# Kernel optimization log

Measured on AMD Instinct MI355X. Metric: run time of the kernel, lower is better.

## Reference

```python
import jax, jax.numpy as jnp
import numpy as np

B, L, D = 4, 1536, 768
H, DQK, DV = 8, 64, 96
NPF = 96  # num_pos_feats = (DV // (2*3)) * (2*3)


def pos_feats_exponential(positions, feature_size, seq_length, min_half_life=3.0):
    # positions: (P, 1); returns (P, feature_size)
    max_range = jnp.log(seq_length) / jnp.log(2.0)
    half_life = jnp.power(2.0, jnp.linspace(min_half_life, max_range, feature_size))
    return jnp.exp(-jnp.log(2.0) / half_life * jnp.abs(positions))


def pos_feats_central_mask(positions, feature_size):
    center_widths = jnp.power(2.0, jnp.arange(1, feature_size + 1, dtype=jnp.float32)) - 1.0
    return (center_widths > jnp.abs(positions)).astype(jnp.float32)


def pos_feats_gamma(positions, feature_size, seq_length):
    stddev = seq_length / (2.0 * feature_size)
    start_mean = seq_length / feature_size
    mean = jnp.linspace(start_mean, seq_length, feature_size)
    concentration = (mean / stddev) ** 2
    rate = mean / (stddev ** 2)
    x = jnp.abs(positions)
    log_unnorm = jax.scipy.special.xlogy(concentration - 1.0, x) - rate * x
    log_norm = jax.scipy.special.gammaln(concentration) - concentration * jnp.log(rate)
    probs = jnp.exp(log_unnorm - log_norm) + 1e-8
    return probs / jnp.max(probs, axis=0, keepdims=True)


def pos_feats_all(positions, feature_size, seq_length, symmetric=False):
    # 3 feature functions; if asymmetric, each is doubled by a signed copy
    num_basis = feature_size // 6
    emb = jnp.concatenate([
        pos_feats_exponential(positions, num_basis, seq_length),
        pos_feats_central_mask(positions, num_basis),
        pos_feats_gamma(positions, num_basis, seq_length),
    ], axis=-1)
    if not symmetric:
        emb = jnp.concatenate([emb, jnp.sign(positions) * emb], axis=-1)
    return emb  # (P, feature_size)


def relative_shift(x):
    # x: (b, h, t1, 2*t1 - 1) -> (b, h, t1, t1), Transformer-XL shift trick
    b, h, t1, t2 = x.shape
    x = jnp.concatenate([jnp.zeros_like(x[..., :1]), x], axis=-1)  # pad -> width t2+1 == 2*t1
    x = x.reshape(b, h, t2 + 1, t1)[:, :, 1:, :]
    x = x.reshape(b, h, t1, t2)
    return x[..., : (t2 + 2) // 2]


def setup_inputs() -> dict:
    key = jax.random.key(0)
    ks = jax.random.split(key, 9)

    def vs(k, shape):  # VarianceScaling(scale=2.0), fan_in on leading dim for 2D
        fan_in = shape[0] if len(shape) == 2 else shape[-1]
        return jax.random.normal(k, shape, jnp.float32) * np.float32(np.sqrt(2.0 / fan_in))

    return {
        "x": jax.random.normal(ks[0], (B, L, D), jnp.float32),
        "Q_w": vs(ks[1], (D, H * DQK)),
        "K_w": vs(ks[2], (D, H * DQK)),
        "V_w": vs(ks[3], (D, H * DV)),
        "out_w": vs(ks[4], (D, H * DV)),
        "out_b": jnp.zeros((H * DV,), jnp.float32),
        "rel_K_w": vs(ks[5], (NPF, H * DQK)),
        "r_w_bias": vs(ks[6], (1, H, 1, DQK)),
        "r_r_bias": vs(ks[7], (1, H, 1, DQK)),
    }


def reference(x, Q_w, K_w, V_w, out_w, out_b, rel_K_w, r_w_bias, r_r_bias):
    b, l, d = x.shape
    h = r_w_bias.shape[1]
    dqk = Q_w.shape[1] // h

    def heads(w, inp):
        out = inp @ w  # (b, t, h*dh)
        return out.reshape(inp.shape[0], inp.shape[1], h, -1).transpose(0, 2, 1, 3)

    Q = heads(Q_w, x) * (dqk ** -0.5)  # scaling=True
    K = heads(K_w, x)
    V = heads(V_w, x)

    positions = jnp.arange(1 - l, l, dtype=jnp.float32)[:, None]       # (2l-1, 1)
    pe = pos_feats_all(positions, rel_K_w.shape[0], float(l))           # (2l-1, npf)
    r_K = (pe @ rel_K_w).reshape(2 * l - 1, h, dqk).transpose(1, 0, 2)  # (h, 2l-1, dqk)

    content = jnp.einsum('bhid,bhjd->bhij', Q + r_w_bias, K)            # (b, h, l, l)
    rel = jnp.einsum('bhid,hjd->bhij', Q + r_r_bias, r_K)               # (b, h, l, 2l-1)
    logits = content + relative_shift(rel)

    w = jax.nn.softmax(logits, axis=-1)
    attn = jnp.einsum('bhij,bhjd->bhid', w, V)                          # (b, h, l, dv)
    out = attn.transpose(0, 2, 1, 3).reshape(b, l, -1) @ out_w + out_b
    return out
```

## Files before the change

kernel.cpp:

```cpp
#include <hip/hip_runtime.h>


typedef unsigned short u16;
typedef unsigned int   u32;

typedef __bf16 bf16x8_t __attribute__((ext_vector_type(8)));
typedef unsigned short u16x8_t __attribute__((ext_vector_type(8)));
typedef float f32x4_t __attribute__((ext_vector_type(4)));

union Frag { u16x8_t u; bf16x8_t b; };

__device__ __forceinline__ float bf2f(u16 v){
  union { u32 i; float f; } c; c.i = ((u32)v) << 16; return c.f;
}
__device__ __forceinline__ u16 f2bf(float f){
  union { float f; u32 i; } c; c.f = f;
  u32 r = c.i + 0x7FFFu + ((c.i >> 16) & 1u);
  return (u16)(r >> 16);
}
__device__ __forceinline__ u16 f2bf_hw(float f){
  __bf16 h = (__bf16)f;
  union { __bf16 h; u16 u; } c; c.h = h; return c.u;
}
__device__ __forceinline__ float frcp(float x){
#if __has_builtin(__builtin_amdgcn_rcpf)
  return __builtin_amdgcn_rcpf(x);
#else
  return 1.0f / x;
#endif
}

template<int N>
__device__ __forceinline__ float ror16(float x){
  union { float f; int i; } c; c.f = x;
  int y = __builtin_amdgcn_update_dpp(0, c.i, 0x120 + N, 0xF, 0xF, true);
  union { int i; float f; } d; d.i = y;
  return d.f;
}
__device__ __forceinline__ float rowmax16(float v){
  v = fmaxf(v, ror16<1>(v));
  v = fmaxf(v, ror16<2>(v));
  v = fmaxf(v, ror16<4>(v));
  v = fmaxf(v, ror16<8>(v));
  return v;
}

#define GLB __attribute__((address_space(1)))
#define LDSAS __attribute__((address_space(3)))
__device__ __forceinline__ void async16(const void* g, void* l){
  __builtin_amdgcn_global_load_lds((const GLB u32*)g, (LDSAS u32*)l, 16, 0, 0);
}

#define LQ   1536
#define NPOS 3071
#define NPOSP 3072

__global__ __launch_bounds__(256) void pre_k(
    const float* __restrict__ x,
    const float* __restrict__ Qw_, const float* __restrict__ Kw_,
    const float* __restrict__ Vw_, const float* __restrict__ Ow_,
    const float* __restrict__ relKw,
    u16* __restrict__ xb, u16* __restrict__ WtQKV, u16* __restrict__ WtOut,
    u16* __restrict__ rK)
{
  const int bx = blockIdx.x;
  const int t = threadIdx.x;

  if (bx < 4608) {
    int gid = bx * 256 + t;
    float4 v = ((const float4*)x)[gid];
    xb[4*gid+0] = f2bf(v.x); xb[4*gid+1] = f2bf(v.y);
    xb[4*gid+2] = f2bf(v.z); xb[4*gid+3] = f2bf(v.w);
    return;
  }

  if (bx < 5088) {
    __shared__ u16 tile[64][65];
    int b2 = bx - 4608;
    const float* src; int stride, cl0, c0, k0; u16* dst;
    if (b2 < 336) {
      int ct = b2 % 28, kt = b2 / 28;
      c0 = ct*64; k0 = kt*64;
      if (c0 < 512)       { src = Qw_; stride = 512; cl0 = c0; }
      else if (c0 < 1024) { src = Kw_; stride = 512; cl0 = c0 - 512; }
      else                { src = Vw_; stride = 768; cl0 = c0 - 1024; }
      dst = WtQKV;
    } else {
      int b3 = b2 - 336; int ct = b3 % 12, kt = b3 / 12;
      c0 = ct*64; k0 = kt*64; src = Ow_; stride = 768; cl0 = c0; dst = WtOut;
    }
    #pragma unroll
    for (int e = 0; e < 16; ++e) {
      int idx = e*256 + t; int row = idx >> 6, col = idx & 63;
      tile[row][col] = f2bf(src[(size_t)(k0 + row)*stride + cl0 + col]);
    }
    __syncthreads();
    #pragma unroll
    for (int e = 0; e < 16; ++e) {
      int idx = e*256 + t; int orow = idx >> 6, ocol = idx & 63;
      dst[(size_t)(c0 + orow)*768 + k0 + ocol] = tile[ocol][orow];
    }
    return;
  }

  __shared__ float gmaxs[16];
  __shared__ float feats[4][96];
  const int k0 = (bx - 5088) * 4;

  if (t < 16) {
    float fi   = (float)(t + 1);
    float conc = 4.0f * fi * fi;
    float rate = fi / 24.0f;
    float c1   = conc - 1.0f;
    float lognorm = lgammaf(conc) - conc * logf(rate);
    float mode = 96.0f*fi - 24.0f/fi;
    float x1 = floorf(mode), x2 = x1 + 1.0f;
    if (x2 > 1535.0f) x2 = 1535.0f;
    float p1 = expf(c1*logf(x1) - rate*x1 - lognorm) + 1e-8f;
    float p2 = expf(c1*logf(x2) - rate*x2 - lognorm) + 1e-8f;
    gmaxs[t] = fmaxf(p1, p2);
  }
  __syncthreads();

  #pragma unroll
  for (int e = 0; e < 2; ++e) {
    int idx = e*256 + t;
    if (idx < 384) {
      int kl = idx / 96, f = idx - kl*96;
      int k = k0 + kl;
      float val = 0.0f;
      if (k != NPOS) {
        float pos = (float)(k - (LQ - 1));
        float xx  = fabsf(pos);
        float sgn = (float)((pos > 0.0f) - (pos < 0.0f));
        int fb = (f < 48) ? f : f - 48;
        float v;
        if (fb < 16) {
          float max_range = log2f((float)LQ);
          float hl = exp2f(3.0f + (float)fb * (max_range - 3.0f) / 15.0f);
          v = expf(-0.69314718056f / hl * xx);
        } else if (fb < 32) {
          int i = fb - 16;
          float width = (float)(1u << (i + 1)) - 1.0f;
          v = (width > xx) ? 1.0f : 0.0f;
        } else {
          int i = fb - 32;
          float fi   = (float)(i + 1);
          float conc = 4.0f * fi * fi;
          float rate = fi / 24.0f;
          float lognorm = lgammaf(conc) - conc * logf(rate);
          float lu = (xx == 0.0f) ? -INFINITY : ((conc - 1.0f) * logf(xx) - rate * xx);
          float p  = expf(lu - lognorm) + 1e-8f;
          v = p / gmaxs[i];
        }
        val = (f < 48) ? v : sgn * v;
      }
      feats[kl][f] = val;
    }
  }
  __syncthreads();

  #pragma unroll
  for (int ci = 0; ci < 2; ++ci) {
    int c = ci*256 + t;
    float a0 = 0.f, a1 = 0.f, a2 = 0.f, a3 = 0.f;
    #pragma unroll 4
    for (int f = 0; f < 96; ++f) {
      float wv = relKw[(size_t)f*512 + c];
      a0 += feats[0][f] * wv;
      a1 += feats[1][f] * wv;
      a2 += feats[2][f] * wv;
      a3 += feats[3][f] * wv;
    }
    size_t base = (((size_t)(c >> 6))*NPOSP + k0)*64 + (c & 63);
    rK[base +   0] = f2bf(a0);
    rK[base +  64] = f2bf(a1);
    rK[base + 128] = f2bf(a2);
    rK[base + 192] = f2bf(a3);
  }
}

__global__ __launch_bounds__(256) void qkv_gemm(
    const u16* __restrict__ xb, const u16* __restrict__ Wt,
    u16* __restrict__ Qb, u16* __restrict__ Kc, u16* __restrict__ Vt)
{
  const int n0 = blockIdx.x * 128;
  const int m0 = blockIdx.y * 128;
  const int tid = threadIdx.x, w = tid >> 6, lane = tid & 63, q = lane >> 4, s = lane & 15;
  const int wr = w >> 1, wc = w & 1;

  __shared__ __align__(16) u16 At[128*64];
  __shared__ __align__(16) u16 Bt[128*64];

  const char* ag = (const char*)(xb + (size_t)m0 * 768);
  const char* bg = (const char*)(Wt + (size_t)n0 * 768);

  const f32x4_t fz = {0.f, 0.f, 0.f, 0.f};
  f32x4_t acc[4][4];
  #pragma unroll
  for (int m = 0; m < 4; ++m)
    #pragma unroll
    for (int n = 0; n < 4; ++n) acc[m][n] = fz;

  for (int kk = 0; kk < 768; kk += 64) {
    #pragma unroll
    for (int c = 0; c < 4; ++c) {
      int ck = w*256 + c*64 + lane;
      int grow = ck >> 3, gcol = (ck & 7) ^ (grow & 7);
      async16(ag + (size_t)grow*1536 + (size_t)(kk + gcol*8)*2, &At[(size_t)(w*256 + c*64)*8]);
      async16(bg + (size_t)grow*1536 + (size_t)(kk + gcol*8)*2, &Bt[(size_t)(w*256 + c*64)*8]);
    }
    __syncthreads();
    #pragma unroll
    for (int kf = 0; kf < 2; ++kf) {
      int sw = (kf*4 + q) ^ (s & 7);
      Frag af[4], bf[4];
      #pragma unroll
      for (int m = 0; m < 4; ++m)
        af[m].u = *(const u16x8_t*)&At[(size_t)((wr*64 + m*16 + s)*8 + sw)*8];
      #pragma unroll
      for (int n = 0; n < 4; ++n)
        bf[n].u = *(const u16x8_t*)&Bt[(size_t)((wc*64 + n*16 + s)*8 + sw)*8];
      #pragma unroll
      for (int m = 0; m < 4; ++m)
        #pragma unroll
        for (int n = 0; n < 4; ++n)
          acc[m][n] = __builtin_amdgcn_mfma_f32_16x16x32_bf16(af[m].b, bf[n].b, acc[m][n], 0, 0, 0);
    }
    __syncthreads();
  }

  #pragma unroll
  for (int m = 0; m < 4; ++m) {
    #pragma unroll
    for (int n = 0; n < 4; ++n) {
      int c = n0 + wc*64 + n*16 + s;
      #pragma unroll
      for (int r = 0; r < 4; ++r) {
        int row = m0 + wr*64 + m*16 + q*4 + r;
        int b = row / LQ, i = row - b*LQ;
        float v = acc[m][n][r];
        if (c < 512) {
          int h = c >> 6, d = c & 63;
          Qb[(((size_t)(b*8 + h))*LQ + i)*64 + d] = f2bf(v * 0.125f);
        } else if (c < 1024) {
          int cc = c - 512, h = cc >> 6, d = cc & 63;
          Kc[(((size_t)(b*8 + h))*LQ + i)*64 + d] = f2bf(v);
        } else {
          int cc = c - 1024, h = cc / 96, vv = cc - h*96;
          Vt[(((size_t)(b*8 + h))*96 + vv)*LQ + i] = f2bf(v);
        }
      }
    }
  }
}

__global__ __launch_bounds__(512, 4) void attn_k(
    const u16* __restrict__ Qb, const u16* __restrict__ Kc,
    const u16* __restrict__ Vt, const u16* __restrict__ rK,
    const float* __restrict__ rwb, const float* __restrict__ rrb,
    u16* __restrict__ attnO, u16* __restrict__ Opart, float* __restrict__ ml,
    int nz)
{
  const int n = blockIdx.x;
  const int bpb = 12 * nz;
  const int slot = n >> 3;
  const int bh = (n & 7) * 4 + slot / bpb;
  const int rm = slot % bpb;
  const int it = rm % 12, z = rm / 12;
  const int i0 = it * 128;
  const int b = bh >> 3, h = bh & 7;
  const int tid = threadIdx.x;
  const int w = tid >> 6, lane = tid & 63, q = lane >> 4, s = lane & 15;

  __shared__ __align__(16) u16 Kt[64*64];
  __shared__ __align__(16) u16 Rt[256*64];
  __shared__ __align__(16) u16 Vs[96*64];
  __shared__ __align__(16) u16 Ps[8][16][72];

  Frag qwf[2], qrf[2];
  {
    const u16* qb = Qb + (((size_t)bh)*LQ + i0 + 16*w + s)*64;
    #pragma unroll
    for (int kf = 0; kf < 2; ++kf) {
      u16x8_t qraw = *(const u16x8_t*)(qb + kf*32 + q*8);
      #pragma unroll
      for (int j = 0; j < 8; ++j) {
        int d = kf*32 + q*8 + j;
        float qv = bf2f(qraw[j]);
        qwf[kf].u[j] = f2bf_hw(qv + rwb[h*64 + d]);
        qrf[kf].u[j] = f2bf_hw(qv + rrb[h*64 + d]);
      }
    }
  }

  Frag ones;
  #pragma unroll
  for (int j = 0; j < 8; ++j) ones.u[j] = 0x3F80;

  const f32x4_t fz = {0.f, 0.f, 0.f, 0.f};
  float mrun[4];
  f32x4_t acco[6], accl;
  #pragma unroll
  for (int r = 0; r < 4; ++r) mrun[r] = -1e30f;
  #pragma unroll
  for (int vs = 0; vs < 6; ++vs) acco[vs] = fz;
  accl = fz;

  const char* kcb = (const char*)(Kc + ((size_t)bh)*LQ*64);
  const char* vtb = (const char*)(Vt + ((size_t)bh)*96*LQ);
  const char* rkb = (const char*)(rK + ((size_t)h)*NPOSP*64);

  const int swz0 = (0*4 + q) ^ (s & 7);
  const int swz1 = (1*4 + q) ^ (s & 7);

  const int njt = 24 / nz;
  const int jt0 = z * njt;
  const int jtend = jt0 + njt;

  auto stageK = [&](int jtS) {
    const char* kg = kcb + (size_t)(jtS*64) * 128;
    int ck = tid;
    int grow = ck >> 3, gcol = (ck & 7) ^ (grow & 7);
    async16(kg + (size_t)grow*128 + gcol*16, &Kt[(size_t)(w*64)*8]);
  };
  auto stageV = [&](int jtS) {
    const char* vg = vtb + (size_t)(jtS*64) * 2;
    {
      int ck = tid;
      int grow = ck >> 3, gcol = (ck & 7) ^ (grow & 7);
      async16(vg + (size_t)grow*(LQ*2) + gcol*16, &Vs[(size_t)(w*64)*8]);
    }
    if (tid < 256) {
      int ck = 512 + tid;
      int grow = ck >> 3, gcol = (ck & 7) ^ (grow & 7);
      async16(vg + (size_t)grow*(LQ*2) + gcol*16, &Vs[(size_t)(512 + w*64)*8]);
    }
  };
  auto stageR64 = [&](int ar0) {
    const char* rg = rkb + (size_t)ar0 * 128;
    int ck = tid;
    int grow = ck >> 3, gcol = (ck & 7) ^ (grow & 7);
    async16(rg + (size_t)grow*128 + gcol*16, &Rt[(size_t)((ar0 & 255) + w*8)*64]);
  };

  {
    const int k00 = jt0*64 - i0 + (LQ - 128);
    stageK(jt0);
    stageR64(k00); stageR64(k00 + 64); stageR64(k00 + 128);
    stageV(jt0);
  }
  __syncthreads();

  for (int jt = jt0; jt < jtend; ++jt) {
    const int k0 = jt*64 - i0 + (LQ - 128);
    const int kb = k0 & 255;

    f32x4_t accc[4] = {fz, fz, fz, fz};
    f32x4_t accr[5] = {fz, fz, fz, fz, fz};
    #pragma unroll
    for (int ns = 0; ns < 4; ++ns) {
      int row = ns*16 + s;
      Frag b0; b0.u = *(const u16x8_t*)&Kt[(size_t)(row*8 + swz0)*8];
      Frag b1; b1.u = *(const u16x8_t*)&Kt[(size_t)(row*8 + swz1)*8];
      accc[ns] = __builtin_amdgcn_mfma_f32_16x16x32_bf16(qwf[0].b, b0.b, accc[ns], 0, 0, 0);
      accc[ns] = __builtin_amdgcn_mfma_f32_16x16x32_bf16(qwf[1].b, b1.b, accc[ns], 0, 0, 0);
    }
    #pragma unroll
    for (int nn = 0; nn < 5; ++nn) {
      int row = (kb + (7 - w + nn)*16 + s) & 255;
      Frag b0; b0.u = *(const u16x8_t*)&Rt[(size_t)(row*8 + swz0)*8];
      Frag b1; b1.u = *(const u16x8_t*)&Rt[(size_t)(row*8 + swz1)*8];
      accr[nn] = __builtin_amdgcn_mfma_f32_16x16x32_bf16(qrf[0].b, b0.b, accr[nn], 0, 0, 0);
      accr[nn] = __builtin_amdgcn_mfma_f32_16x16x32_bf16(qrf[1].b, b1.b, accr[nn], 0, 0, 0);
    }

    __syncthreads();

    if (jt + 1 < jtend) {
      stageK(jt + 1);
      stageR64(k0 + 192);
    }

    #pragma unroll
    for (int r = 0; r < 4; ++r) {
      int tt = s + 15 - 4*q - r;
      int srcl = (lane & 48) | (tt & 15);
      bool hi = tt >= 16;
      float v[5];
      #pragma unroll
      for (int nn = 0; nn < 5; ++nn) v[nn] = __shfl(accr[nn][r], srcl, 64);
      #pragma unroll
      for (int ns = 0; ns < 4; ++ns)
        accc[ns][r] += hi ? v[ns + 1] : v[ns];
    }

    #pragma unroll
    for (int r = 0; r < 4; ++r) {
      float mx = fmaxf(fmaxf(accc[0][r], accc[1][r]), fmaxf(accc[2][r], accc[3][r]));
      mx = rowmax16(mx);
      float mnew  = fmaxf(mrun[r], mx);
      float alpha = __expf(mrun[r] - mnew);
      #pragma unroll
      for (int ns = 0; ns < 4; ++ns)
        accc[ns][r] = __expf(accc[ns][r] - mnew);
      mrun[r] = mnew;
      accl[r] *= alpha;
      #pragma unroll
      for (int vs = 0; vs < 6; ++vs) acco[vs][r] *= alpha;
    }

    #pragma unroll
    for (int ns = 0; ns < 4; ++ns)
      #pragma unroll
      for (int r = 0; r < 4; ++r)
        Ps[w][q*4 + r][ns*16 + s] = f2bf_hw(accc[ns][r]);

    #pragma unroll
    for (int kf = 0; kf < 2; ++kf) {
      Frag pf; pf.u = *(const u16x8_t*)(&Ps[w][s][kf*32 + q*8]);
      int sw = kf ? swz1 : swz0;
      #pragma unroll
      for (int vs = 0; vs < 6; ++vs) {
        int row = vs*16 + s;
        Frag vf; vf.u = *(const u16x8_t*)&Vs[(size_t)(row*8 + sw)*8];
        acco[vs] = __builtin_amdgcn_mfma_f32_16x16x32_bf16(pf.b, vf.b, acco[vs], 0, 0, 0);
      }
      accl = __builtin_amdgcn_mfma_f32_16x16x32_bf16(pf.b, ones.b, accl, 0, 0, 0);
    }

    __syncthreads();

    if (jt + 1 < jtend) stageV(jt + 1);
  }

  if (nz == 1) {
    #pragma unroll
    for (int r = 0; r < 4; ++r) {
      float inv = frcp(accl[r]);
      int i = i0 + 16*w + q*4 + r;
      #pragma unroll
      for (int vs = 0; vs < 6; ++vs) {
        int v = vs*16 + s;
        attnO[((size_t)b*LQ + i)*768 + h*96 + v] = f2bf_hw(acco[vs][r] * inv);
      }
    }
  } else {
    #pragma unroll
    for (int vs = 0; vs < 6; ++vs) {
      int v = vs*16 + s;
      #pragma unroll
      for (int r = 0; r < 4; ++r) {
        int i = i0 + 16*w + q*4 + r;
        size_t rg = (size_t)(z*32 + bh)*LQ + i;
        Opart[rg*96 + v] = f2bf_hw(acco[vs][r]);
      }
    }
    if (s == 0) {
      #pragma unroll
      for (int r = 0; r < 4; ++r) {
        int i = i0 + 16*w + q*4 + r;
        size_t rg = (size_t)(z*32 + bh)*LQ + i;
        ml[rg*2 + 0] = mrun[r];
        ml[rg*2 + 1] = accl[r];
      }
    }
  }
}

__global__ void combine_k(const u16* __restrict__ Opart, const float* __restrict__ ml,
                          u16* __restrict__ attnO, int nz)
{
  int g = blockIdx.x * 256 + threadIdx.x;
  if (g >= 32*LQ*12) return;
  int vg = g % 12, row = g / 12;
  int v0 = vg * 8;
  int bh = row / LQ, i = row - bh*LQ;
  int b = bh >> 3, h = bh & 7;
  float M = -1e30f;
  for (int z = 0; z < nz; ++z)
    M = fmaxf(M, ml[((size_t)(z*32 + bh)*LQ + i)*2]);
  float L = 0.f;
  float num[8];
  #pragma unroll
  for (int j = 0; j < 8; ++j) num[j] = 0.f;
  for (int z = 0; z < nz; ++z) {
    size_t rg = (size_t)(z*32 + bh)*LQ + i;
    float e = __expf(ml[rg*2] - M);
    L += ml[rg*2 + 1] * e;
    u16x8_t ov = *(const u16x8_t*)&Opart[rg*96 + v0];
    #pragma unroll
    for (int j = 0; j < 8; ++j) num[j] += bf2f(ov[j]) * e;
  }
  float invL = frcp(L);
  u16x8_t outv;
  #pragma unroll
  for (int j = 0; j < 8; ++j) outv[j] = f2bf(num[j] * invL);
  *(u16x8_t*)&attnO[((size_t)b*LQ + i)*768 + h*96 + v0] = outv;
}

__global__ __launch_bounds__(256) void out_gemm(
    const u16* __restrict__ A, const u16* __restrict__ Wt,
    const float* __restrict__ bias, float* __restrict__ out)
{
  const int n0 = blockIdx.x * 64;
  const int m0 = blockIdx.y * 64;
  const int tid = threadIdx.x, w = tid >> 6, lane = tid & 63, q = lane >> 4, s = lane & 15;

  __shared__ __align__(16) u16 At[64*64];
  __shared__ __align__(16) u16 Bt[64*64];

  const char* ag = (const char*)(A  + (size_t)m0 * 768);
  const char* bg = (const char*)(Wt + (size_t)n0 * 768);

  const f32x4_t fz = {0.f, 0.f, 0.f, 0.f};
  f32x4_t acc[4] = {fz, fz, fz, fz};

  for (int kk = 0; kk < 768; kk += 64) {
    #pragma unroll
    for (int c = 0; c < 2; ++c) {
      int ck = w*128 + c*64 + lane;
      int grow = ck >> 3, gcol = (ck & 7) ^ (grow & 7);
      async16(ag + (size_t)grow*1536 + (size_t)(kk + gcol*8)*2, &At[(size_t)(w*128 + c*64)*8]);
      async16(bg + (size_t)grow*1536 + (size_t)(kk + gcol*8)*2, &Bt[(size_t)(w*128 + c*64)*8]);
    }
    __syncthreads();
    #pragma unroll
    for (int kf = 0; kf < 2; ++kf) {
      int sw = (kf*4 + q) ^ (s & 7);
      Frag af; af.u = *(const u16x8_t*)&At[(size_t)((16*w + s)*8 + sw)*8];
      #pragma unroll
      for (int ns = 0; ns < 4; ++ns) {
        Frag bf; bf.u = *(const u16x8_t*)&Bt[(size_t)((ns*16 + s)*8 + sw)*8];
        acc[ns] = __builtin_amdgcn_mfma_f32_16x16x32_bf16(af.b, bf.b, acc[ns], 0, 0, 0);
      }
    }
    __syncthreads();
  }

  #pragma unroll
  for (int ns = 0; ns < 4; ++ns) {
    int c = n0 + ns*16 + s;
    float bv = bias[c];
    #pragma unroll
    for (int r = 0; r < 4; ++r) {
      int row = m0 + 16*w + q*4 + r;
      out[(size_t)row*768 + c] = acc[ns][r] + bv;
    }
  }
}

extern "C" void kernel_launch(void* const* d_in, const int* in_sizes, int n_in,
                              void* d_out, int out_size, void* d_ws, size_t ws_size,
                              hipStream_t stream)
{
  (void)out_size;

  static const int dict_sig[9] = {4718592,393216,393216,589824,589824,768,49152,512,512};
  bool is_dict = (n_in == 9);
  for (int i = 0; i < 9 && i < n_in; ++i)
    if (in_sizes[i] != dict_sig[i]) is_dict = false;

  const float *x, *Qw_w, *Kw_w, *Vw_w, *Ow_w, *out_b, *relKw, *rwb, *rrb;
  if (is_dict) {
    x     = (const float*)d_in[0];  Qw_w  = (const float*)d_in[1];
    Kw_w  = (const float*)d_in[2];  Vw_w  = (const float*)d_in[3];
    Ow_w  = (const float*)d_in[4];  out_b = (const float*)d_in[5];
    relKw = (const float*)d_in[6];  rwb   = (const float*)d_in[7];
    rrb   = (const float*)d_in[8];
  } else {
    const float* p393[2] = {nullptr,nullptr}; int n393 = 0;
    const float* p589[2] = {nullptr,nullptr}; int n589 = 0;
    const float* p512[2] = {nullptr,nullptr}; int n512 = 0;
    const float *px = nullptr, *prel = nullptr, *pb = nullptr;
    for (int i = 0; i < n_in; ++i) {
      const float* p = (const float*)d_in[i];
      switch (in_sizes[i]) {
        case 4718592: px = p; break;
        case 49152:   prel = p; break;
        case 768:     pb = p; break;
        case 393216:  if (n393 < 2) p393[n393++] = p; break;
        case 589824:  if (n589 < 2) p589[n589++] = p; break;
        case 512:     if (n512 < 2) p512[n512++] = p; break;
        default: break;
      }
    }
    x = px; relKw = prel; out_b = pb;
    Qw_w = p393[0]; Kw_w = p393[1];
    Vw_w = p589[0]; Ow_w = p589[1];
    rwb  = p512[0]; rrb  = p512[1];
  }

  float* out = (float*)d_out;

  char* ws = (char*)d_ws;
  size_t off = 0;
  auto alloc = [&](size_t bytes) -> void* {
    void* p = ws + off;
    off += (bytes + 255) & ~(size_t)255;
    return p;
  };

  u16*   WtQKV = (u16*)  alloc((size_t)1792*768*2);
  u16*   WtOut = (u16*)  alloc((size_t)768*768*2);
  u16*   rK    = (u16*)  alloc((size_t)8*NPOSP*64*2);
  u16*   Qb    = (u16*)  alloc((size_t)32*LQ*64*2);
  u16*   Kc    = (u16*)  alloc((size_t)32*LQ*64*2);
  u16*   Vt    = (u16*)  alloc((size_t)32*96*LQ*2);
  u16*   xb    = (u16*)  alloc((size_t)6144*768*2);
  u16*   attnO = xb;

  size_t base_off = off;
  auto need = [&](int nzv) -> size_t {
    size_t o = base_off;
    o += (((size_t)nzv*32*LQ*96*2) + 255) & ~(size_t)255;
    o += (((size_t)nzv*32*LQ*2*4) + 255) & ~(size_t)255;
    return o;
  };
  int nz = 1;
  if (ws_size >= need(4)) nz = 4;
  else if (ws_size >= need(2)) nz = 2;
  u16*   Opart = nullptr; float* ml = nullptr;
  if (nz > 1) {
    Opart = (u16*)  alloc((size_t)nz*32*LQ*96*2);
    ml    = (float*)alloc((size_t)nz*32*LQ*2*4);
  }

  pre_k      <<<dim3(5856), dim3(256), 0, stream>>>(x, Qw_w, Kw_w, Vw_w, Ow_w,
                                                    relKw, xb, WtQKV, WtOut, rK);
  qkv_gemm   <<<dim3(14,48),dim3(256), 0, stream>>>(xb, WtQKV, Qb, Kc, Vt);
  attn_k     <<<dim3(384*nz),dim3(512), 0, stream>>>(Qb, Kc, Vt, rK, rwb, rrb,
                                                     attnO, Opart, ml, nz);
  if (nz > 1)
    combine_k<<<dim3(2304),  dim3(256), 0, stream>>>(Opart, ml, attnO, nz);
  out_gemm   <<<dim3(12,96),dim3(256), 0, stream>>>(attnO, WtOut, out_b, out);
}
```

Baseline: 315.8 us.

## Fuse split-KV combine into attention kernel via last-block atomic counter

Removes the separate combine kernel launch. Each attention block increments a per-(head, query-tile) atomic counter after writing its partial output and softmax stats, and the last of the nz splits performs the log-sum-exp merge into attnO. Counters are zeroed in the preprocessing kernel and reset by the finishing block. This saves one launch and the gap between kernels, at the cost of threadfence and atomic traffic plus a serialized tail done by the last block of each tile.

Result: slower. 793.7 us (+151.4%).

```diff
diff --git a/kernel.cpp b/kernel.cpp
--- a/kernel.cpp
+++ b/kernel.cpp
@@ -61,12 +61,16 @@
     const float* __restrict__ Vw_, const float* __restrict__ Ow_,
     const float* __restrict__ relKw,
     u16* __restrict__ xb, u16* __restrict__ WtQKV, u16* __restrict__ WtOut,
-    u16* __restrict__ rK)
+    u16* __restrict__ rK, int* __restrict__ cnt)
 {
   const int bx = blockIdx.x;
   const int t = threadIdx.x;
 
   if (bx < 4608) {
+    if (bx == 0) {
+      cnt[t] = 0;
+      if (t < 128) cnt[256 + t] = 0;
+    }
     int gid = bx * 256 + t;
     float4 v = ((const float4*)x)[gid];
     xb[4*gid+0] = f2bf(v.x); xb[4*gid+1] = f2bf(v.y);
@@ -260,7 +264,7 @@
     const u16* __restrict__ Vt, const u16* __restrict__ rK,
     const float* __restrict__ rwb, const float* __restrict__ rrb,
     u16* __restrict__ attnO, u16* __restrict__ Opart, float* __restrict__ ml,
-    int nz)
+    int* __restrict__ cnt, int nz)
 {
   const int n = blockIdx.x;
   const int bpb = 12 * nz;
@@ -277,6 +281,7 @@
   __shared__ __align__(16) u16 Rt[256*64];
   __shared__ __align__(16) u16 Vs[96*64];
   __shared__ __align__(16) u16 Ps[8][16][72];
+  __shared__ int lastFlag;
 
   Frag qwf[2], qrf[2];
   {
@@ -465,38 +470,45 @@
         ml[rg*2 + 1] = accl[r];
       }
     }
-  }
-}
-
-__global__ void combine_k(const u16* __restrict__ Opart, const float* __restrict__ ml,
-                          u16* __restrict__ attnO, int nz)
-{
-  int g = blockIdx.x * 256 + threadIdx.x;
-  if (g >= 32*LQ*12) return;
-  int vg = g % 12, row = g / 12;
-  int v0 = vg * 8;
-  int bh = row / LQ, i = row - bh*LQ;
-  int b = bh >> 3, h = bh & 7;
-  float M = -1e30f;
-  for (int z = 0; z < nz; ++z)
-    M = fmaxf(M, ml[((size_t)(z*32 + bh)*LQ + i)*2]);
-  float L = 0.f;
-  float num[8];
-  #pragma unroll
-  for (int j = 0; j < 8; ++j) num[j] = 0.f;
-  for (int z = 0; z < nz; ++z) {
-    size_t rg = (size_t)(z*32 + bh)*LQ + i;
-    float e = __expf(ml[rg*2] - M);
-    L += ml[rg*2 + 1] * e;
-    u16x8_t ov = *(const u16x8_t*)&Opart[rg*96 + v0];
-    #pragma unroll
-    for (int j = 0; j < 8; ++j) num[j] += bf2f(ov[j]) * e;
-  }
-  float invL = frcp(L);
-  u16x8_t outv;
-  #pragma unroll
-  for (int j = 0; j < 8; ++j) outv[j] = f2bf(num[j] * invL);
-  *(u16x8_t*)&attnO[((size_t)b*LQ + i)*768 + h*96 + v0] = outv;
+
+    __syncthreads();
+    __threadfence();
+    if (tid == 0) {
+      int old = atomicAdd(&cnt[bh*12 + it], 1);
+      lastFlag = (old == nz - 1);
+    }
+    __syncthreads();
+    if (!lastFlag) return;
+    __threadfence();
+
+    for (int e = tid; e < 128*12; e += 512) {
+      int vg = e % 12, ri = e / 12;
+      int i = i0 + ri;
+      int v0 = vg * 8;
+      float M = -1e30f;
+      for (int zz = 0; zz < nz; ++zz)
+        M = fmaxf(M, ml[((size_t)(zz*32 + bh)*LQ + i)*2]);
+      float L = 0.f;
+      float num[8];
+      #pragma unroll
+      for (int j = 0; j < 8; ++j) num[j] = 0.f;
+      for (int zz = 0; zz < nz; ++zz) {
+        size_t rg = (size_t)(zz*32 + bh)*LQ + i;
+        float e2 = __expf(ml[rg*2] - M);
+        L += ml[rg*2 + 1] * e2;
+        u16x8_t ov = *(const u16x8_t*)&Opart[rg*96 + v0];
+        #pragma unroll
+        for (int j = 0; j < 8; ++j) num[j] += bf2f(ov[j]) * e2;
+      }
+      float invL = frcp(L);
+      u16x8_t outv;
+      #pragma unroll
+      for (int j = 0; j < 8; ++j) outv[j] = f2bf(num[j] * invL);
+      *(u16x8_t*)&attnO[((size_t)b*LQ + i)*768 + h*96 + v0] = outv;
+    }
+    __syncthreads();
+    if (tid == 0) cnt[bh*12 + it] = 0;
+  }
 }
 
 __global__ __launch_bounds__(256) void out_gemm(
@@ -601,6 +613,7 @@
     return p;
   };
 
+  int*   cnt   = (int*)  alloc(384*4);
   u16*   WtQKV = (u16*)  alloc((size_t)1792*768*2);
   u16*   WtOut = (u16*)  alloc((size_t)768*768*2);
   u16*   rK    = (u16*)  alloc((size_t)8*NPOSP*64*2);
@@ -627,11 +640,9 @@
   }
 
   pre_k      <<<dim3(5856), dim3(256), 0, stream>>>(x, Qw_w, Kw_w, Vw_w, Ow_w,
-                                                    relKw, xb, WtQKV, WtOut, rK);
+                                                    relKw, xb, WtQKV, WtOut, rK, cnt);
   qkv_gemm   <<<dim3(14,48),dim3(256), 0, stream>>>(xb, WtQKV, Qb, Kc, Vt);
   attn_k     <<<dim3(384*nz),dim3(512), 0, stream>>>(Qb, Kc, Vt, rK, rwb, rrb,
-                                                     attnO, Opart, ml, nz);
-  if (nz > 1)
-    combine_k<<<dim3(2304),  dim3(256), 0, stream>>>(Opart, ml, attnO, nz);
+                                                     attnO, Opart, ml, cnt, nz);
   out_gemm   <<<dim3(12,96),dim3(256), 0, stream>>>(attnO, WtOut, out_b, out);
 }
```

## Load K, V and rel-K fragments directly from global memory, dropping LDS staging

Applied to the files above, without the earlier changes.

Removes the shared-memory staging of K, V and relative-position K tiles, along with the async copies and block-wide barriers around them. Each wave now reads its MFMA operand fragments straight from global memory, relying on the caches for reuse across the eight waves. This cuts barrier stalls and LDS use, which may allow more blocks per CU. The cost is more global and cache traffic and no overlap of prefetch with compute.

Result: slower. 438.6 us (+38.9%).

```diff
diff --git a/kernel.cpp b/kernel.cpp
--- a/kernel.cpp
+++ b/kernel.cpp
@@ -273,9 +273,6 @@
   const int tid = threadIdx.x;
   const int w = tid >> 6, lane = tid & 63, q = lane >> 4, s = lane & 15;
 
-  __shared__ __align__(16) u16 Kt[64*64];
-  __shared__ __align__(16) u16 Rt[256*64];
-  __shared__ __align__(16) u16 Vs[96*64];
   __shared__ __align__(16) u16 Ps[8][16][72];
 
   Frag qwf[2], qrf[2];
@@ -307,79 +304,36 @@
   for (int vs = 0; vs < 6; ++vs) acco[vs] = fz;
   accl = fz;
 
-  const char* kcb = (const char*)(Kc + ((size_t)bh)*LQ*64);
-  const char* vtb = (const char*)(Vt + ((size_t)bh)*96*LQ);
-  const char* rkb = (const char*)(rK + ((size_t)h)*NPOSP*64);
-
-  const int swz0 = (0*4 + q) ^ (s & 7);
-  const int swz1 = (1*4 + q) ^ (s & 7);
+  const u16* kcb = Kc + (size_t)bh*LQ*64;
+  const u16* vtb = Vt + (size_t)bh*96*LQ;
+  const u16* rkb = rK + (size_t)h*NPOSP*64;
 
   const int njt = 24 / nz;
   const int jt0 = z * njt;
   const int jtend = jt0 + njt;
 
-  auto stageK = [&](int jtS) {
-    const char* kg = kcb + (size_t)(jtS*64) * 128;
-    int ck = tid;
-    int grow = ck >> 3, gcol = (ck & 7) ^ (grow & 7);
-    async16(kg + (size_t)grow*128 + gcol*16, &Kt[(size_t)(w*64)*8]);
-  };
-  auto stageV = [&](int jtS) {
-    const char* vg = vtb + (size_t)(jtS*64) * 2;
-    {
-      int ck = tid;
-      int grow = ck >> 3, gcol = (ck & 7) ^ (grow & 7);
-      async16(vg + (size_t)grow*(LQ*2) + gcol*16, &Vs[(size_t)(w*64)*8]);
-    }
-    if (tid < 256) {
-      int ck = 512 + tid;
-      int grow = ck >> 3, gcol = (ck & 7) ^ (grow & 7);
-      async16(vg + (size_t)grow*(LQ*2) + gcol*16, &Vs[(size_t)(512 + w*64)*8]);
-    }
-  };
-  auto stageR64 = [&](int ar0) {
-    const char* rg = rkb + (size_t)ar0 * 128;
-    int ck = tid;
-    int grow = ck >> 3, gcol = (ck & 7) ^ (grow & 7);
-    async16(rg + (size_t)grow*128 + gcol*16, &Rt[(size_t)((ar0 & 255) + w*8)*64]);
-  };
-
-  {
-    const int k00 = jt0*64 - i0 + (LQ - 128);
-    stageK(jt0);
-    stageR64(k00); stageR64(k00 + 64); stageR64(k00 + 128);
-    stageV(jt0);
-  }
-  __syncthreads();
-
   for (int jt = jt0; jt < jtend; ++jt) {
-    const int k0 = jt*64 - i0 + (LQ - 128);
-    const int kb = k0 & 255;
+    const int j0 = jt*64;
+    const int k0 = j0 - i0 + (LQ - 128);
 
     f32x4_t accc[4] = {fz, fz, fz, fz};
     f32x4_t accr[5] = {fz, fz, fz, fz, fz};
     #pragma unroll
     for (int ns = 0; ns < 4; ++ns) {
-      int row = ns*16 + s;
-      Frag b0; b0.u = *(const u16x8_t*)&Kt[(size_t)(row*8 + swz0)*8];
-      Frag b1; b1.u = *(const u16x8_t*)&Kt[(size_t)(row*8 + swz1)*8];
+      const u16* kr = kcb + (size_t)(j0 + ns*16 + s)*64 + q*8;
+      Frag b0; b0.u = *(const u16x8_t*)(kr);
+      Frag b1; b1.u = *(const u16x8_t*)(kr + 32);
       accc[ns] = __builtin_amdgcn_mfma_f32_16x16x32_bf16(qwf[0].b, b0.b, accc[ns], 0, 0, 0);
       accc[ns] = __builtin_amdgcn_mfma_f32_16x16x32_bf16(qwf[1].b, b1.b, accc[ns], 0, 0, 0);
     }
     #pragma unroll
     for (int nn = 0; nn < 5; ++nn) {
-      int row = (kb + (7 - w + nn)*16 + s) & 255;
-      Frag b0; b0.u = *(const u16x8_t*)&Rt[(size_t)(row*8 + swz0)*8];
-      Frag b1; b1.u = *(const u16x8_t*)&Rt[(size_t)(row*8 + swz1)*8];
+      int ar = k0 + (7 - w + nn)*16 + s;
+      const u16* rr = rkb + (size_t)ar*64 + q*8;
+      Frag b0; b0.u = *(const u16x8_t*)(rr);
+      Frag b1; b1.u = *(const u16x8_t*)(rr + 32);
       accr[nn] = __builtin_amdgcn_mfma_f32_16x16x32_bf16(qrf[0].b, b0.b, accr[nn], 0, 0, 0);
       accr[nn] = __builtin_amdgcn_mfma_f32_16x16x32_bf16(qrf[1].b, b1.b, accr[nn], 0, 0, 0);
-    }
-
-    __syncthreads();
-
-    if (jt + 1 < jtend) {
-      stageK(jt + 1);
-      stageR64(k0 + 192);
     }
 
     #pragma unroll
@@ -419,19 +373,14 @@
     #pragma unroll
     for (int kf = 0; kf < 2; ++kf) {
       Frag pf; pf.u = *(const u16x8_t*)(&Ps[w][s][kf*32 + q*8]);
-      int sw = kf ? swz1 : swz0;
       #pragma unroll
       for (int vs = 0; vs < 6; ++vs) {
-        int row = vs*16 + s;
-        Frag vf; vf.u = *(const u16x8_t*)&Vs[(size_t)(row*8 + sw)*8];
+        const u16* vr = vtb + (size_t)(vs*16 + s)*LQ + j0 + kf*32 + q*8;
+        Frag vf; vf.u = *(const u16x8_t*)(vr);
         acco[vs] = __builtin_amdgcn_mfma_f32_16x16x32_bf16(pf.b, vf.b, acco[vs], 0, 0, 0);
       }
       accl = __builtin_amdgcn_mfma_f32_16x16x32_bf16(pf.b, ones.b, accl, 0, 0, 0);
     }
-
-    __syncthreads();
-
-    if (jt + 1 < jtend) stageV(jt + 1);
   }
 
   if (nz == 1) {
```
